# Optimization experiments

Measured on AMD Instinct MI355X. Metric: run time of the kernel, lower is better.

Reference implementation:

```python
import jax, jax.numpy as jnp
import numpy as np

N, E, D, ATT = 20000, 5000, 128, 32
NUM_LAYERS = 4
LN_EPS = 1e-5
DEG_EPS = 1e-12

def setup_inputs() -> dict:
    key = jax.random.key(0)
    k1, k2, k3, k4 = jax.random.split(key, 4)
    node_embeddings = jax.random.normal(k1, (N, D), dtype=jnp.float32)
    hypergraph_matrix = (jax.random.uniform(k2, (N, E)) < 0.01).astype(jnp.float32)
    ln_gamma = jnp.ones((D,), jnp.float32)
    ln_beta = jnp.zeros((D,), jnp.float32)
    W_att = jax.random.normal(k3, (D, ATT), dtype=jnp.float32) * (1.0 / np.sqrt(D))
    b_att = jnp.zeros((ATT,), jnp.float32)
    q_att = jax.random.normal(k4, (ATT,), dtype=jnp.float32)
    return {"node_embeddings": node_embeddings, "hypergraph_matrix": hypergraph_matrix,
            "ln_gamma": ln_gamma, "ln_beta": ln_beta,
            "W_att": W_att, "b_att": b_att, "q_att": q_att}

def _layernorm(y, gamma, beta):
    mu = jnp.mean(y, axis=-1, keepdims=True)
    var = jnp.mean(jnp.square(y - mu), axis=-1, keepdims=True)
    return (y - mu) * jax.lax.rsqrt(var + LN_EPS) * gamma + beta

def reference(node_embeddings, hypergraph_matrix, ln_gamma, ln_beta, W_att, b_att, q_att):
    H = hypergraph_matrix                      # [N, E]
    dv_inv = 1.0 / jnp.maximum(jnp.sum(H, axis=1), DEG_EPS)   # [N]
    de_inv = 1.0 / jnp.maximum(jnp.sum(H, axis=0), DEG_EPS)   # [E]
    x = node_embeddings
    for _ in range(NUM_LAYERS):
        edge_mean = (H.T @ x) * de_inv[:, None]       # V->E mean, [E, D]
        node_msg = (H @ edge_mean) * dv_inv[:, None]  # E->V mean, [N, D]
        x = _layernorm(node_msg + node_embeddings, ln_gamma, ln_beta)
        # dropout(p=0.35) is identity in eval mode
    # per-edge masked mean over member nodes (vectorized segment-mean)
    M = (H > 0).astype(x.dtype)                        # [N, E]
    cnt = jnp.maximum(jnp.sum(M, axis=0), 1.0)         # [E]
    edge_out = (M.T @ x) / cnt[:, None]                # [E, D]
    # dot-product attention pooling over hyperedges
    scores = jax.nn.softmax(jnp.tanh(edge_out @ W_att + b_att) @ q_att)  # [E]
    return scores @ edge_out                           # [D]
```

## Files before the change

kernel.cpp:

```cpp
#include <hip/hip_runtime.h>
#include <hip/hip_fp16.h>
#include <math.h>

#define NN 20000
#define EE 5000
#define DD 128
#define ATT 32
#define NUM_LAYERS 4
#define LN_EPS 1e-5f
#define DEG_EPS 1e-12f

#define ECAP 320
#define NCAP 128
#define CSTRIDE 32

typedef float vfloat4 __attribute__((ext_vector_type(4)));

__device__ inline unsigned pack2h(float x, float y) {
    return __builtin_bit_cast(unsigned, __floats2half2_rn(x, y));
}
__device__ inline void acc8(float* a, uint4 u) {
    __half2 h;
    h = __builtin_bit_cast(__half2, u.x); a[0] += __low2float(h); a[1] += __high2float(h);
    h = __builtin_bit_cast(__half2, u.y); a[2] += __low2float(h); a[3] += __high2float(h);
    h = __builtin_bit_cast(__half2, u.z); a[4] += __low2float(h); a[5] += __high2float(h);
    h = __builtin_bit_cast(__half2, u.w); a[6] += __low2float(h); a[7] += __high2float(h);
}

__global__ __launch_bounds__(256) void build_adj(
    const float* __restrict__ H, int* __restrict__ cur, int* __restrict__ nc,
    int* __restrict__ el, int* __restrict__ nl,
    const float* __restrict__ x0, __half* __restrict__ xh0) {
    const int n = blockIdx.x;
    const int tid = threadIdx.x;
    __shared__ int lcnt;
    __shared__ int lbuf[NCAP];
    if (tid == 0) lcnt = 0;
    __syncthreads();
    const vfloat4* row = reinterpret_cast<const vfloat4*>(H + (size_t)n * EE);
    for (int i = tid; i < EE / 4; i += 256) {
        const vfloat4 h = __builtin_nontemporal_load(row + i);
        float v[4] = {h.x, h.y, h.z, h.w};
        const int ebase = i * 4;
#pragma unroll
        for (int k = 0; k < 4; k++) {
            if (v[k] != 0.0f) {
                int s = atomicAdd(&lcnt, 1);
                if (s < NCAP) lbuf[s] = ebase + k;
            }
        }
    }
    __syncthreads();
    const int c = min(lcnt, NCAP);
    for (int k = tid; k < c; k += 256) {
        const int e = lbuf[k];
        nl[(size_t)n * NCAP + k] = e;
        const int slot = atomicAdd(&cur[e << 5], 1);
        if (slot < ECAP) el[(size_t)e * ECAP + slot] = n;
    }
    if (tid < 64) {
        const float2 v = reinterpret_cast<const float2*>(x0 + (size_t)n * DD)[tid];
        reinterpret_cast<unsigned*>(xh0 + (size_t)n * DD)[tid] = pack2h(v.x, v.y);
    }
    if (tid == 0) nc[n] = lcnt;
}

template <bool FINAL>
__global__ __launch_bounds__(256) void edge_gather16(
    const __half* __restrict__ xh, const int* __restrict__ cur,
    const int* __restrict__ el, __half* __restrict__ outh,
    float* __restrict__ eout, const float* __restrict__ W,
    const float* __restrict__ bb, const float* __restrict__ qv,
    float* __restrict__ t) {
    __shared__ int ilst[ECAP];
    __shared__ float part[4][16][8];
    __shared__ float rowbuf[DD];
    const int e = blockIdx.x;
    const int tid = threadIdx.x;
    const int cnt = cur[e << 5];
    const int c = min(cnt, ECAP);
    const int* lst = el + (size_t)e * ECAP;
    for (int k = tid; k < c; k += 256) ilst[k] = lst[k];
    __syncthreads();
    const int lane16 = tid & 15;
    const int s = tid >> 4;
    const int wave = tid >> 6;
    float a[8] = {0, 0, 0, 0, 0, 0, 0, 0};
    float b[8] = {0, 0, 0, 0, 0, 0, 0, 0};
    int i = s;
    for (; i + 48 < c; i += 64) {
        const int n0 = ilst[i];
        const int n1 = ilst[i + 16];
        const int n2 = ilst[i + 32];
        const int n3 = ilst[i + 48];
        const uint4 u0 = *reinterpret_cast<const uint4*>(xh + n0 * DD + lane16 * 8);
        const uint4 u1 = *reinterpret_cast<const uint4*>(xh + n1 * DD + lane16 * 8);
        const uint4 u2 = *reinterpret_cast<const uint4*>(xh + n2 * DD + lane16 * 8);
        const uint4 u3 = *reinterpret_cast<const uint4*>(xh + n3 * DD + lane16 * 8);
        acc8(a, u0); acc8(b, u1); acc8(a, u2); acc8(b, u3);
    }
    for (; i + 16 < c; i += 32) {
        const int n0 = ilst[i];
        const int n1 = ilst[i + 16];
        const uint4 u0 = *reinterpret_cast<const uint4*>(xh + n0 * DD + lane16 * 8);
        const uint4 u1 = *reinterpret_cast<const uint4*>(xh + n1 * DD + lane16 * 8);
        acc8(a, u0); acc8(b, u1);
    }
    if (i < c) {
        acc8(a, *reinterpret_cast<const uint4*>(xh + ilst[i] * DD + lane16 * 8));
    }
#pragma unroll
    for (int k = 0; k < 8; k++) {
        float v = a[k] + b[k];
        v += __shfl_down(v, 16);
        v += __shfl_down(v, 32);
        a[k] = v;
    }
    if ((tid & 63) < 16) {
#pragma unroll
        for (int k = 0; k < 8; k++) part[wave][lane16][k] = a[k];
    }
    __syncthreads();
    if (tid < 16) {
        const float inv = 1.0f / fmaxf((float)cnt, DEG_EPS);
        float o[8];
#pragma unroll
        for (int k = 0; k < 8; k++)
            o[k] = (part[0][tid][k] + part[1][tid][k] + part[2][tid][k] + part[3][tid][k]) * inv;
        if (!FINAL) {
            uint4 u;
            u.x = pack2h(o[0], o[1]); u.y = pack2h(o[2], o[3]);
            u.z = pack2h(o[4], o[5]); u.w = pack2h(o[6], o[7]);
            *reinterpret_cast<uint4*>(outh + e * DD + tid * 8) = u;
        } else {
#pragma unroll
            for (int k = 0; k < 8; k++) rowbuf[tid * 8 + k] = o[k];
            *reinterpret_cast<float4*>(eout + e * DD + tid * 8) =
                make_float4(o[0], o[1], o[2], o[3]);
            *reinterpret_cast<float4*>(eout + e * DD + tid * 8 + 4) =
                make_float4(o[4], o[5], o[6], o[7]);
        }
    }
    if (FINAL) {
        __syncthreads();
        float r = 0.0f;
        if (tid < ATT) {
            float acc = 0.0f;
#pragma unroll 4
            for (int d = 0; d < DD; d++) acc += rowbuf[d] * W[d * ATT + tid];
            r = tanhf(acc + bb[tid]) * qv[tid];
        }
        for (int off = 16; off > 0; off >>= 1) r += __shfl_down(r, off);
        if (tid == 0) t[e] = r;
    }
}

__global__ __launch_bounds__(128) void node_gather_ln16(
    const __half* __restrict__ emean, const int* __restrict__ nc,
    const int* __restrict__ nl, const float* __restrict__ x0,
    const float* __restrict__ gamma, const float* __restrict__ beta,
    __half* __restrict__ xout) {
    __shared__ int ilst[NCAP];
    __shared__ float part[2][16][8];
    const int n = blockIdx.x;
    const int tid = threadIdx.x;
    const int cnt = nc[n];
    const int c = min(cnt, NCAP);
    const int* lst = nl + (size_t)n * NCAP;
    if (tid < c) ilst[tid] = lst[tid];
    __syncthreads();
    const int lane16 = tid & 15;
    const int s = tid >> 4;
    const int wave = tid >> 6;
    float a[8] = {0, 0, 0, 0, 0, 0, 0, 0};
    float b[8] = {0, 0, 0, 0, 0, 0, 0, 0};
    int i = s;
    for (; i + 24 < c; i += 32) {
        const int e0 = ilst[i];
        const int e1 = ilst[i + 8];
        const int e2 = ilst[i + 16];
        const int e3 = ilst[i + 24];
        const uint4 u0 = *reinterpret_cast<const uint4*>(emean + e0 * DD + lane16 * 8);
        const uint4 u1 = *reinterpret_cast<const uint4*>(emean + e1 * DD + lane16 * 8);
        const uint4 u2 = *reinterpret_cast<const uint4*>(emean + e2 * DD + lane16 * 8);
        const uint4 u3 = *reinterpret_cast<const uint4*>(emean + e3 * DD + lane16 * 8);
        acc8(a, u0); acc8(b, u1); acc8(a, u2); acc8(b, u3);
    }
    for (; i + 8 < c; i += 16) {
        const int e0 = ilst[i];
        const int e1 = ilst[i + 8];
        const uint4 u0 = *reinterpret_cast<const uint4*>(emean + e0 * DD + lane16 * 8);
        const uint4 u1 = *reinterpret_cast<const uint4*>(emean + e1 * DD + lane16 * 8);
        acc8(a, u0); acc8(b, u1);
    }
    if (i < c) {
        acc8(a, *reinterpret_cast<const uint4*>(emean + ilst[i] * DD + lane16 * 8));
    }
#pragma unroll
    for (int k = 0; k < 8; k++) {
        float v = a[k] + b[k];
        v += __shfl_down(v, 16);
        v += __shfl_down(v, 32);
        a[k] = v;
    }
    if ((tid & 63) < 16) {
#pragma unroll
        for (int k = 0; k < 8; k++) part[wave][lane16][k] = a[k];
    }
    __syncthreads();
    if (tid < 16) {
        const float inv = 1.0f / fmaxf((float)cnt, DEG_EPS);
        const float4 x0a = *reinterpret_cast<const float4*>(x0 + n * DD + tid * 8);
        const float4 x0b = *reinterpret_cast<const float4*>(x0 + n * DD + tid * 8 + 4);
        float y[8];
        y[0] = (part[0][tid][0] + part[1][tid][0]) * inv + x0a.x;
        y[1] = (part[0][tid][1] + part[1][tid][1]) * inv + x0a.y;
        y[2] = (part[0][tid][2] + part[1][tid][2]) * inv + x0a.z;
        y[3] = (part[0][tid][3] + part[1][tid][3]) * inv + x0a.w;
        y[4] = (part[0][tid][4] + part[1][tid][4]) * inv + x0b.x;
        y[5] = (part[0][tid][5] + part[1][tid][5]) * inv + x0b.y;
        y[6] = (part[0][tid][6] + part[1][tid][6]) * inv + x0b.z;
        y[7] = (part[0][tid][7] + part[1][tid][7]) * inv + x0b.w;
        float sm = 0.0f, ss = 0.0f;
#pragma unroll
        for (int k = 0; k < 8; k++) { sm += y[k]; ss += y[k] * y[k]; }
        for (int off = 8; off > 0; off >>= 1) {
            sm += __shfl_down(sm, off);
            ss += __shfl_down(ss, off);
        }
        sm = __shfl(sm, 0);
        ss = __shfl(ss, 0);
        const float mu = sm * (1.0f / 128.0f);
        float var = ss * (1.0f / 128.0f) - mu * mu;
        var = fmaxf(var, 0.0f);
        const float rstd = 1.0f / sqrtf(var + LN_EPS);
        const float4 g0 = *reinterpret_cast<const float4*>(gamma + tid * 8);
        const float4 g1 = *reinterpret_cast<const float4*>(gamma + tid * 8 + 4);
        const float4 b0 = *reinterpret_cast<const float4*>(beta + tid * 8);
        const float4 b1 = *reinterpret_cast<const float4*>(beta + tid * 8 + 4);
        float gg[8] = {g0.x, g0.y, g0.z, g0.w, g1.x, g1.y, g1.z, g1.w};
        float bb[8] = {b0.x, b0.y, b0.z, b0.w, b1.x, b1.y, b1.z, b1.w};
        float o[8];
#pragma unroll
        for (int k = 0; k < 8; k++) o[k] = (y[k] - mu) * rstd * gg[k] + bb[k];
        uint4 u;
        u.x = pack2h(o[0], o[1]); u.y = pack2h(o[2], o[3]);
        u.z = pack2h(o[4], o[5]); u.w = pack2h(o[6], o[7]);
        *reinterpret_cast<uint4*>(xout + n * DD + tid * 8) = u;
    }
}

__global__ __launch_bounds__(1024) void softmax_stats(
    const float* __restrict__ t, float* __restrict__ MS) {
    __shared__ float red[16];
    __shared__ float smax;
    const int tid = threadIdx.x;
    const int wid = tid >> 6;
    float m = -1e30f;
    for (int i = tid; i < EE; i += 1024) m = fmaxf(m, t[i]);
    for (int off = 32; off > 0; off >>= 1) m = fmaxf(m, __shfl_down(m, off));
    if ((tid & 63) == 0) red[wid] = m;
    __syncthreads();
    if (tid < 64) {
        float v = (tid < 16) ? red[tid] : -1e30f;
        for (int off = 8; off > 0; off >>= 1) v = fmaxf(v, __shfl_down(v, off));
        if (tid == 0) smax = v;
    }
    __syncthreads();
    const float M = smax;
    float sum = 0.0f;
    for (int i = tid; i < EE; i += 1024) sum += expf(t[i] - M);
    for (int off = 32; off > 0; off >>= 1) sum += __shfl_down(sum, off);
    if ((tid & 63) == 0) red[wid] = sum;
    __syncthreads();
    if (tid < 64) {
        float v = (tid < 16) ? red[tid] : 0.0f;
        for (int off = 8; off > 0; off >>= 1) v += __shfl_down(v, off);
        if (tid == 0) { MS[0] = M; MS[1] = v; }
    }
}

__global__ __launch_bounds__(128) void weighted_sum(
    const float* __restrict__ eout, const float* __restrict__ t,
    const float* __restrict__ MS, float* __restrict__ out) {
    const int d = threadIdx.x;
    const float M = MS[0];
    const float invS = 1.0f / MS[1];
    float acc = 0.0f;
    for (int e = blockIdx.x; e < EE; e += gridDim.x) {
        const float w = expf(t[e] - M);
        acc += w * eout[e * DD + d];
    }
    atomicAdd(&out[d], acc * invS);
}

extern "C" void kernel_launch(void* const* d_in, const int* in_sizes, int n_in,
                              void* d_out, int out_size, void* d_ws, size_t ws_size,
                              hipStream_t stream) {
    const float* x0 = (const float*)d_in[0];
    const float* H = (const float*)d_in[1];
    const float* gamma = (const float*)d_in[2];
    const float* beta = (const float*)d_in[3];
    const float* W = (const float*)d_in[4];
    const float* b = (const float*)d_in[5];
    const float* qv = (const float*)d_in[6];
    float* out = (float*)d_out;

    char* w = (char*)d_ws;
    int* cur = (int*)w;       w += (size_t)EE * CSTRIDE * 4;
    int* nc = (int*)w;        w += (size_t)NN * 4;
    int* el = (int*)w;        w += (size_t)EE * ECAP * 4;
    int* nl = (int*)w;        w += (size_t)NN * NCAP * 4;
    __half* xh0 = (__half*)w; w += (size_t)NN * DD * 2;
    __half* xA = (__half*)w;  w += (size_t)NN * DD * 2;
    __half* xB = (__half*)w;  w += (size_t)NN * DD * 2;
    __half* emean = (__half*)w; w += (size_t)EE * DD * 2;
    float* eout = (float*)w;  w += (size_t)EE * DD * 4;
    float* t = (float*)w;     w += (size_t)EE * 4;
    float* MS = (float*)w;    w += 16;

    hipMemsetAsync(cur, 0, (size_t)EE * CSTRIDE * 4, stream);
    hipMemsetAsync(d_out, 0, (size_t)DD * sizeof(float), stream);

    build_adj<<<NN, 256, 0, stream>>>(H, cur, nc, el, nl, x0, xh0);

    const __half* xin = xh0;
    __half* bufs[2] = {xA, xB};
    for (int l = 0; l < NUM_LAYERS; l++) {
        edge_gather16<false><<<EE, 256, 0, stream>>>(
            xin, cur, el, emean, nullptr, nullptr, nullptr, nullptr, nullptr);
        node_gather_ln16<<<NN, 128, 0, stream>>>(
            emean, nc, nl, x0, gamma, beta, bufs[l & 1]);
        xin = bufs[l & 1];
    }

    edge_gather16<true><<<EE, 256, 0, stream>>>(
        xin, cur, el, nullptr, eout, W, b, qv, t);
    softmax_stats<<<1, 1024, 0, stream>>>(t, MS);
    weighted_sum<<<256, 128, 0, stream>>>(eout, t, MS, out);
}
```

Baseline: 730.6 us.

## Fuse all stages into one persistent cooperative kernel with grid syncs

Replaces the chain of roughly 12 kernel launches (adjacency build, four edge/node gather layers, final edge pass, softmax stats, weighted sum) with a single persistent cooperative kernel. The stages are separated by grid.sync and each block walks its work with a grid-stride loop. The intent is to remove per-launch overhead and the gaps between kernels. The trade-offs are grid-wide barrier cost, a grid capped at 1024 blocks with fewer waves in flight, and a serial softmax step on block 0. The old multi-kernel path is kept as a fallback if the cooperative launch fails.

```diff
diff --git a/kernel.cpp b/kernel.cpp
--- a/kernel.cpp
+++ b/kernel.cpp
@@ -1,6 +1,9 @@
 #include <hip/hip_runtime.h>
 #include <hip/hip_fp16.h>
+#include <hip/hip_cooperative_groups.h>
 #include <math.h>
+
+namespace cg = cooperative_groups;
 
 #define NN 20000
 #define EE 5000
@@ -25,6 +28,296 @@
     h = __builtin_bit_cast(__half2, u.y); a[2] += __low2float(h); a[3] += __high2float(h);
     h = __builtin_bit_cast(__half2, u.z); a[4] += __low2float(h); a[5] += __high2float(h);
     h = __builtin_bit_cast(__half2, u.w); a[6] += __low2float(h); a[7] += __high2float(h);
+}
+
+
+template <bool FINAL>
+__device__ __forceinline__ void edge_phase(
+    const __half* __restrict__ xh, const int* __restrict__ cur,
+    const int* __restrict__ el, __half* __restrict__ outh,
+    float* __restrict__ eout, const float* __restrict__ W,
+    const float* __restrict__ bb, const float* __restrict__ qv,
+    float* __restrict__ t, int* ilst, float (*part)[16][8], float* rowbuf) {
+    const int tid = threadIdx.x;
+    const int lane16 = tid & 15;
+    const int s = tid >> 4;
+    const int wave = tid >> 6;
+    for (int e = blockIdx.x; e < EE; e += gridDim.x) {
+        __syncthreads();
+        const int cnt = cur[e << 5];
+        const int c = min(cnt, ECAP);
+        const int* lst = el + (size_t)e * ECAP;
+        for (int k = tid; k < c; k += 256) ilst[k] = lst[k];
+        __syncthreads();
+        float a[8] = {0, 0, 0, 0, 0, 0, 0, 0};
+        float b[8] = {0, 0, 0, 0, 0, 0, 0, 0};
+        int i = s;
+        for (; i + 48 < c; i += 64) {
+            const int n0 = ilst[i];
+            const int n1 = ilst[i + 16];
+            const int n2 = ilst[i + 32];
+            const int n3 = ilst[i + 48];
+            const uint4 u0 = *reinterpret_cast<const uint4*>(xh + n0 * DD + lane16 * 8);
+            const uint4 u1 = *reinterpret_cast<const uint4*>(xh + n1 * DD + lane16 * 8);
+            const uint4 u2 = *reinterpret_cast<const uint4*>(xh + n2 * DD + lane16 * 8);
+            const uint4 u3 = *reinterpret_cast<const uint4*>(xh + n3 * DD + lane16 * 8);
+            acc8(a, u0); acc8(b, u1); acc8(a, u2); acc8(b, u3);
+        }
+        for (; i + 16 < c; i += 32) {
+            const int n0 = ilst[i];
+            const int n1 = ilst[i + 16];
+            const uint4 u0 = *reinterpret_cast<const uint4*>(xh + n0 * DD + lane16 * 8);
+            const uint4 u1 = *reinterpret_cast<const uint4*>(xh + n1 * DD + lane16 * 8);
+            acc8(a, u0); acc8(b, u1);
+        }
+        if (i < c) {
+            acc8(a, *reinterpret_cast<const uint4*>(xh + ilst[i] * DD + lane16 * 8));
+        }
+#pragma unroll
+        for (int k = 0; k < 8; k++) {
+            float v = a[k] + b[k];
+            v += __shfl_down(v, 16);
+            v += __shfl_down(v, 32);
+            a[k] = v;
+        }
+        if ((tid & 63) < 16) {
+#pragma unroll
+            for (int k = 0; k < 8; k++) part[wave][lane16][k] = a[k];
+        }
+        __syncthreads();
+        if (tid < 16) {
+            const float inv = 1.0f / fmaxf((float)cnt, DEG_EPS);
+            float o[8];
+#pragma unroll
+            for (int k = 0; k < 8; k++)
+                o[k] = (part[0][tid][k] + part[1][tid][k] + part[2][tid][k] + part[3][tid][k]) * inv;
+            if (!FINAL) {
+                uint4 u;
+                u.x = pack2h(o[0], o[1]); u.y = pack2h(o[2], o[3]);
+                u.z = pack2h(o[4], o[5]); u.w = pack2h(o[6], o[7]);
+                *reinterpret_cast<uint4*>(outh + e * DD + tid * 8) = u;
+            } else {
+#pragma unroll
+                for (int k = 0; k < 8; k++) rowbuf[tid * 8 + k] = o[k];
+                *reinterpret_cast<float4*>(eout + e * DD + tid * 8) =
+                    make_float4(o[0], o[1], o[2], o[3]);
+                *reinterpret_cast<float4*>(eout + e * DD + tid * 8 + 4) =
+                    make_float4(o[4], o[5], o[6], o[7]);
+            }
+        }
+        if (FINAL) {
+            __syncthreads();
+            float r = 0.0f;
+            if (tid < ATT) {
+                float acc = 0.0f;
+#pragma unroll 4
+                for (int d = 0; d < DD; d++) acc += rowbuf[d] * W[d * ATT + tid];
+                r = tanhf(acc + bb[tid]) * qv[tid];
+            }
+            for (int off = 16; off > 0; off >>= 1) r += __shfl_down(r, off);
+            if (tid == 0) t[e] = r;
+        }
+    }
+}
+
+__global__ __launch_bounds__(256, 4) void mega(
+    const float* __restrict__ x0, const float* __restrict__ H,
+    const float* __restrict__ gamma, const float* __restrict__ beta,
+    const float* __restrict__ W, const float* __restrict__ bb,
+    const float* __restrict__ qv,
+    int* __restrict__ cur, int* __restrict__ nc,
+    int* __restrict__ el, int* __restrict__ nl,
+    __half* __restrict__ xh0, __half* __restrict__ xA, __half* __restrict__ xB,
+    __half* __restrict__ emean, float* __restrict__ eout,
+    float* __restrict__ t, float* __restrict__ MS, float* __restrict__ out) {
+    cg::grid_group grid = cg::this_grid();
+    const int tid = threadIdx.x;
+
+    __shared__ int s_ilst[ECAP];
+    __shared__ float s_part[4][16][8];
+    __shared__ float s_rowbuf[DD];
+    __shared__ int s_lcnt;
+
+    for (int n = blockIdx.x; n < NN; n += gridDim.x) {
+        __syncthreads();
+        if (tid == 0) s_lcnt = 0;
+        __syncthreads();
+        const vfloat4* row = reinterpret_cast<const vfloat4*>(H + (size_t)n * EE);
+        for (int i = tid; i < EE / 4; i += 256) {
+            const vfloat4 h = __builtin_nontemporal_load(row + i);
+            float v[4] = {h.x, h.y, h.z, h.w};
+            const int ebase = i * 4;
+#pragma unroll
+            for (int k = 0; k < 4; k++) {
+                if (v[k] != 0.0f) {
+                    int sl = atomicAdd(&s_lcnt, 1);
+                    if (sl < NCAP) s_ilst[sl] = ebase + k;
+                }
+            }
+        }
+        __syncthreads();
+        const int cnt = s_lcnt;
+        const int c = min(cnt, NCAP);
+        for (int k = tid; k < c; k += 256) {
+            const int e = s_ilst[k];
+            nl[(size_t)n * NCAP + k] = e;
+            const int slot = atomicAdd(&cur[e << 5], 1);
+            if (slot < ECAP) el[(size_t)e * ECAP + slot] = n;
+        }
+        if (tid < 64) {
+            const float2 v = reinterpret_cast<const float2*>(x0 + (size_t)n * DD)[tid];
+            reinterpret_cast<unsigned*>(xh0 + (size_t)n * DD)[tid] = pack2h(v.x, v.y);
+        }
+        if (tid == 0) nc[n] = cnt;
+    }
+    grid.sync();
+
+    const __half* xin = xh0;
+    for (int l = 0; l < NUM_LAYERS; l++) {
+        edge_phase<false>(xin, cur, el, emean, nullptr, nullptr, nullptr, nullptr,
+                          nullptr, s_ilst, s_part, s_rowbuf);
+        grid.sync();
+
+        {
+            int (*nilst)[NCAP] = reinterpret_cast<int (*)[NCAP]>(s_ilst);
+            float (*npart)[2][16][8] = reinterpret_cast<float (*)[2][16][8]>(s_part);
+            __half* xout = (l & 1) ? xB : xA;
+            const int half = tid >> 7;
+            const int ltid = tid & 127;
+            const int lane16 = ltid & 15;
+            const int s = ltid >> 4;
+            const int wv = ltid >> 6;
+            for (int nb = blockIdx.x * 2; nb < NN; nb += gridDim.x * 2) {
+                const int n = nb + half;
+                __syncthreads();
+                const int cnt = nc[n];
+                const int c = min(cnt, NCAP);
+                const int* lst = nl + (size_t)n * NCAP;
+                if (ltid < c) nilst[half][ltid] = lst[ltid];
+                __syncthreads();
+                float a[8] = {0, 0, 0, 0, 0, 0, 0, 0};
+                float b[8] = {0, 0, 0, 0, 0, 0, 0, 0};
+                int i = s;
+                for (; i + 24 < c; i += 32) {
+                    const int e0 = nilst[half][i];
+                    const int e1 = nilst[half][i + 8];
+                    const int e2 = nilst[half][i + 16];
+                    const int e3 = nilst[half][i + 24];
+                    const uint4 u0 = *reinterpret_cast<const uint4*>(emean + e0 * DD + lane16 * 8);
+                    const uint4 u1 = *reinterpret_cast<const uint4*>(emean + e1 * DD + lane16 * 8);
+                    const uint4 u2 = *reinterpret_cast<const uint4*>(emean + e2 * DD + lane16 * 8);
+                    const uint4 u3 = *reinterpret_cast<const uint4*>(emean + e3 * DD + lane16 * 8);
+                    acc8(a, u0); acc8(b, u1); acc8(a, u2); acc8(b, u3);
+                }
+                for (; i + 8 < c; i += 16) {
+                    const int e0 = nilst[half][i];
+                    const int e1 = nilst[half][i + 8];
+                    const uint4 u0 = *reinterpret_cast<const uint4*>(emean + e0 * DD + lane16 * 8);
+                    const uint4 u1 = *reinterpret_cast<const uint4*>(emean + e1 * DD + lane16 * 8);
+                    acc8(a, u0); acc8(b, u1);
+                }
+                if (i < c) {
+                    acc8(a, *reinterpret_cast<const uint4*>(emean + nilst[half][i] * DD + lane16 * 8));
+                }
+#pragma unroll
+                for (int k = 0; k < 8; k++) {
+                    float v = a[k] + b[k];
+                    v += __shfl_down(v, 16);
+                    v += __shfl_down(v, 32);
+                    a[k] = v;
+                }
+                if ((ltid & 63) < 16) {
+#pragma unroll
+                    for (int k = 0; k < 8; k++) npart[half][wv][lane16][k] = a[k];
+                }
+                __syncthreads();
+                if (ltid < 16) {
+                    const float inv = 1.0f / fmaxf((float)cnt, DEG_EPS);
+                    const float4 x0a = *reinterpret_cast<const float4*>(x0 + n * DD + ltid * 8);
+                    const float4 x0b = *reinterpret_cast<const float4*>(x0 + n * DD + ltid * 8 + 4);
+                    float y[8];
+                    y[0] = (npart[half][0][ltid][0] + npart[half][1][ltid][0]) * inv + x0a.x;
+                    y[1] = (npart[half][0][ltid][1] + npart[half][1][ltid][1]) * inv + x0a.y;
+                    y[2] = (npart[half][0][ltid][2] + npart[half][1][ltid][2]) * inv + x0a.z;
+                    y[3] = (npart[half][0][ltid][3] + npart[half][1][ltid][3]) * inv + x0a.w;
+                    y[4] = (npart[half][0][ltid][4] + npart[half][1][ltid][4]) * inv + x0b.x;
+                    y[5] = (npart[half][0][ltid][5] + npart[half][1][ltid][5]) * inv + x0b.y;
+                    y[6] = (npart[half][0][ltid][6] + npart[half][1][ltid][6]) * inv + x0b.z;
+                    y[7] = (npart[half][0][ltid][7] + npart[half][1][ltid][7]) * inv + x0b.w;
+                    float sm = 0.0f, ss = 0.0f;
+#pragma unroll
+                    for (int k = 0; k < 8; k++) { sm += y[k]; ss += y[k] * y[k]; }
+                    for (int off = 8; off > 0; off >>= 1) {
+                        sm += __shfl_down(sm, off);
+                        ss += __shfl_down(ss, off);
+                    }
+                    sm = __shfl(sm, 0);
+                    ss = __shfl(ss, 0);
+                    const float mu = sm * (1.0f / 128.0f);
+                    float var = ss * (1.0f / 128.0f) - mu * mu;
+                    var = fmaxf(var, 0.0f);
+                    const float rstd = 1.0f / sqrtf(var + LN_EPS);
+                    const float4 g0 = *reinterpret_cast<const float4*>(gamma + ltid * 8);
+                    const float4 g1 = *reinterpret_cast<const float4*>(gamma + ltid * 8 + 4);
+                    const float4 b0 = *reinterpret_cast<const float4*>(beta + ltid * 8);
+                    const float4 b1 = *reinterpret_cast<const float4*>(beta + ltid * 8 + 4);
+                    float gg[8] = {g0.x, g0.y, g0.z, g0.w, g1.x, g1.y, g1.z, g1.w};
+                    float bv[8] = {b0.x, b0.y, b0.z, b0.w, b1.x, b1.y, b1.z, b1.w};
+                    float o[8];
+#pragma unroll
+                    for (int k = 0; k < 8; k++) o[k] = (y[k] - mu) * rstd * gg[k] + bv[k];
+                    uint4 u;
+                    u.x = pack2h(o[0], o[1]); u.y = pack2h(o[2], o[3]);
+                    u.z = pack2h(o[4], o[5]); u.w = pack2h(o[6], o[7]);
+                    *reinterpret_cast<uint4*>(xout + n * DD + ltid * 8) = u;
+                }
+            }
+        }
+        grid.sync();
+        xin = (l & 1) ? xB : xA;
+    }
+
+    edge_phase<true>(xin, cur, el, nullptr, eout, W, bb, qv, t,
+                     s_ilst, s_part, s_rowbuf);
+    grid.sync();
+
+    if (blockIdx.x == 0) {
+        __syncthreads();
+        float m = -1e30f;
+        for (int i = tid; i < EE; i += 256) m = fmaxf(m, t[i]);
+        for (int off = 32; off > 0; off >>= 1) m = fmaxf(m, __shfl_down(m, off));
+        if ((tid & 63) == 0) s_rowbuf[tid >> 6] = m;
+        __syncthreads();
+        if (tid == 0) {
+            s_rowbuf[8] = fmaxf(fmaxf(s_rowbuf[0], s_rowbuf[1]),
+                                fmaxf(s_rowbuf[2], s_rowbuf[3]));
+        }
+        __syncthreads();
+        const float M = s_rowbuf[8];
+        float sum = 0.0f;
+        for (int i = tid; i < EE; i += 256) sum += expf(t[i] - M);
+        for (int off = 32; off > 0; off >>= 1) sum += __shfl_down(sum, off);
+        if ((tid & 63) == 0) s_rowbuf[16 + (tid >> 6)] = sum;
+        __syncthreads();
+        if (tid == 0) {
+            MS[0] = M;
+            MS[1] = s_rowbuf[16] + s_rowbuf[17] + s_rowbuf[18] + s_rowbuf[19];
+        }
+    }
+    grid.sync();
+
+    {
+        const int WS = min((int)gridDim.x, 256);
+        if (blockIdx.x < WS && tid < 128) {
+            const float M = MS[0];
+            const float invS = 1.0f / MS[1];
+            float acc = 0.0f;
+            for (int e = blockIdx.x; e < EE; e += WS) {
+                acc += expf(t[e] - M) * eout[e * DD + tid];
+            }
+            atomicAdd(&out[tid], acc * invS);
+        }
+    }
 }
 
 __global__ __launch_bounds__(256) void build_adj(
@@ -75,8 +368,8 @@
     __shared__ int ilst[ECAP];
     __shared__ float part[4][16][8];
     __shared__ float rowbuf[DD];
+    const int tid = threadIdx.x;
     const int e = blockIdx.x;
-    const int tid = threadIdx.x;
     const int cnt = cur[e << 5];
     const int c = min(cnt, ECAP);
     const int* lst = el + (size_t)e * ECAP;
@@ -322,20 +615,41 @@
     hipMemsetAsync(cur, 0, (size_t)EE * CSTRIDE * 4, stream);
     hipMemsetAsync(d_out, 0, (size_t)DD * sizeof(float), stream);
 
-    build_adj<<<NN, 256, 0, stream>>>(H, cur, nc, el, nl, x0, xh0);
-
-    const __half* xin = xh0;
-    __half* bufs[2] = {xA, xB};
-    for (int l = 0; l < NUM_LAYERS; l++) {
-        edge_gather16<false><<<EE, 256, 0, stream>>>(
-            xin, cur, el, emean, nullptr, nullptr, nullptr, nullptr, nullptr);
-        node_gather_ln16<<<NN, 128, 0, stream>>>(
-            emean, nc, nl, x0, gamma, beta, bufs[l & 1]);
-        xin = bufs[l & 1];
-    }
-
-    edge_gather16<true><<<EE, 256, 0, stream>>>(
-        xin, cur, el, nullptr, eout, W, b, qv, t);
-    softmax_stats<<<1, 1024, 0, stream>>>(t, MS);
-    weighted_sum<<<256, 128, 0, stream>>>(eout, t, MS, out);
-}
+    static int grid = 0;
+    if (grid == 0) {
+        int mb = 0;
+        if (hipOccupancyMaxActiveBlocksPerMultiprocessor(&mb, mega, 256, 0)
+                != hipSuccess || mb <= 0)
+            mb = 4;
+        grid = mb * 256;
+        if (grid > 1024) grid = 1024;
+        if (grid < 256) grid = 256;
+    }
+
+    void* args[] = {(void*)&x0, (void*)&H, (void*)&gamma, (void*)&beta,
+                    (void*)&W, (void*)&b, (void*)&qv,
+                    (void*)&cur, (void*)&nc, (void*)&el, (void*)&nl,
+                    (void*)&xh0, (void*)&xA, (void*)&xB,
+                    (void*)&emean, (void*)&eout, (void*)&t, (void*)&MS,
+                    (void*)&out};
+    hipError_t err = hipLaunchCooperativeKernel(
+        mega, dim3(grid), dim3(256), args, 0, stream);
+
+    if (err != hipSuccess) {
+        (void)hipGetLastError();
+        build_adj<<<NN, 256, 0, stream>>>(H, cur, nc, el, nl, x0, xh0);
+        const __half* xin = xh0;
+        __half* bufs[2] = {xA, xB};
+        for (int l = 0; l < NUM_LAYERS; l++) {
+            edge_gather16<false><<<EE, 256, 0, stream>>>(
+                xin, cur, el, emean, nullptr, nullptr, nullptr, nullptr, nullptr);
+            node_gather_ln16<<<NN, 128, 0, stream>>>(
+                emean, nc, nl, x0, gamma, beta, bufs[l & 1]);
+            xin = bufs[l & 1];
+        }
+        edge_gather16<true><<<EE, 256, 0, stream>>>(
+            xin, cur, el, nullptr, eout, W, b, qv, t);
+        softmax_stats<<<1, 1024, 0, stream>>>(t, MS);
+        weighted_sum<<<256, 128, 0, stream>>>(eout, t, MS, out);
+    }
+}
```

Result: slower. 1.730 ms (+136.8%).

## Split node features into lo/hi half planes and split edge gather per half

Applied to the files above, without the earlier changes.

Stores the fp16 node feature matrix as two separate planes of 64 columns each, written by build_adj and node_gather_ln16. The per-layer edge gather now launches twice as many blocks, each summing only one half of the feature columns over a smaller 1.6 MB plane, with blocks ordered so the two halves of neighbouring edges are interleaved. The aim is better L2 locality on the random gathers and more parallelism. In exchange, each block reloads the edge's member list, and every gathered row read is only 128 bytes.

```diff
diff --git a/kernel.cpp b/kernel.cpp
--- a/kernel.cpp
+++ b/kernel.cpp
@@ -27,10 +27,12 @@
     h = __builtin_bit_cast(__half2, u.w); a[6] += __low2float(h); a[7] += __high2float(h);
 }
 
+
 __global__ __launch_bounds__(256) void build_adj(
     const float* __restrict__ H, int* __restrict__ cur, int* __restrict__ nc,
     int* __restrict__ el, int* __restrict__ nl,
-    const float* __restrict__ x0, __half* __restrict__ xh0) {
+    const float* __restrict__ x0, __half* __restrict__ xlo0,
+    __half* __restrict__ xhi0) {
     const int n = blockIdx.x;
     const int tid = threadIdx.x;
     __shared__ int lcnt;
@@ -60,15 +62,88 @@
     }
     if (tid < 64) {
         const float2 v = reinterpret_cast<const float2*>(x0 + (size_t)n * DD)[tid];
-        reinterpret_cast<unsigned*>(xh0 + (size_t)n * DD)[tid] = pack2h(v.x, v.y);
+        const unsigned u = pack2h(v.x, v.y);
+        if (tid < 32)
+            reinterpret_cast<unsigned*>(xlo0 + (size_t)n * 64)[tid] = u;
+        else
+            reinterpret_cast<unsigned*>(xhi0 + (size_t)n * 64)[tid - 32] = u;
     }
     if (tid == 0) nc[n] = lcnt;
 }
 
-template <bool FINAL>
-__global__ __launch_bounds__(256) void edge_gather16(
-    const __half* __restrict__ xh, const int* __restrict__ cur,
-    const int* __restrict__ el, __half* __restrict__ outh,
+__global__ __launch_bounds__(256) void edge_gather_half(
+    const __half* __restrict__ xlo, const __half* __restrict__ xhi,
+    const int* __restrict__ cur, const int* __restrict__ el,
+    __half* __restrict__ emean) {
+    __shared__ int ilst[ECAP];
+    __shared__ float part[4][8][8];
+    const int b = blockIdx.x;
+    const int g = b & 7;
+    const int half = g >> 2;
+    const int e = (b >> 3) * 4 + (g & 3);
+    const int tid = threadIdx.x;
+    const int cnt = cur[e << 5];
+    const int c = min(cnt, ECAP);
+    const int* lst = el + (size_t)e * ECAP;
+    for (int k = tid; k < c; k += 256) ilst[k] = lst[k];
+    __syncthreads();
+    const __half* xt = half ? xhi : xlo;
+    const int lane8 = tid & 7;
+    const int s = tid >> 3;
+    const int wave = tid >> 6;
+    float a[8] = {0, 0, 0, 0, 0, 0, 0, 0};
+    float bacc[8] = {0, 0, 0, 0, 0, 0, 0, 0};
+    int i = s;
+    for (; i + 96 < c; i += 128) {
+        const int n0 = ilst[i];
+        const int n1 = ilst[i + 32];
+        const int n2 = ilst[i + 64];
+        const int n3 = ilst[i + 96];
+        const uint4 u0 = *reinterpret_cast<const uint4*>(xt + n0 * 64 + lane8 * 8);
+        const uint4 u1 = *reinterpret_cast<const uint4*>(xt + n1 * 64 + lane8 * 8);
+        const uint4 u2 = *reinterpret_cast<const uint4*>(xt + n2 * 64 + lane8 * 8);
+        const uint4 u3 = *reinterpret_cast<const uint4*>(xt + n3 * 64 + lane8 * 8);
+        acc8(a, u0); acc8(bacc, u1); acc8(a, u2); acc8(bacc, u3);
+    }
+    for (; i + 32 < c; i += 64) {
+        const int n0 = ilst[i];
+        const int n1 = ilst[i + 32];
+        const uint4 u0 = *reinterpret_cast<const uint4*>(xt + n0 * 64 + lane8 * 8);
+        const uint4 u1 = *reinterpret_cast<const uint4*>(xt + n1 * 64 + lane8 * 8);
+        acc8(a, u0); acc8(bacc, u1);
+    }
+    if (i < c) {
+        acc8(a, *reinterpret_cast<const uint4*>(xt + ilst[i] * 64 + lane8 * 8));
+    }
+#pragma unroll
+    for (int k = 0; k < 8; k++) {
+        float v = a[k] + bacc[k];
+        v += __shfl_down(v, 8);
+        v += __shfl_down(v, 16);
+        v += __shfl_down(v, 32);
+        a[k] = v;
+    }
+    if ((tid & 63) < 8) {
+#pragma unroll
+        for (int k = 0; k < 8; k++) part[wave][lane8][k] = a[k];
+    }
+    __syncthreads();
+    if (tid < 8) {
+        const float inv = 1.0f / fmaxf((float)cnt, DEG_EPS);
+        float o[8];
+#pragma unroll
+        for (int k = 0; k < 8; k++)
+            o[k] = (part[0][tid][k] + part[1][tid][k] + part[2][tid][k] + part[3][tid][k]) * inv;
+        uint4 u;
+        u.x = pack2h(o[0], o[1]); u.y = pack2h(o[2], o[3]);
+        u.z = pack2h(o[4], o[5]); u.w = pack2h(o[6], o[7]);
+        *reinterpret_cast<uint4*>(emean + (size_t)e * DD + half * 64 + tid * 8) = u;
+    }
+}
+
+__global__ __launch_bounds__(256) void edge_final(
+    const __half* __restrict__ xlo, const __half* __restrict__ xhi,
+    const int* __restrict__ cur, const int* __restrict__ el,
     float* __restrict__ eout, const float* __restrict__ W,
     const float* __restrict__ bb, const float* __restrict__ qv,
     float* __restrict__ t) {
@@ -85,6 +160,7 @@
     const int lane16 = tid & 15;
     const int s = tid >> 4;
     const int wave = tid >> 6;
+    const __half* base = ((lane16 < 8) ? xlo : xhi) + (lane16 & 7) * 8;
     float a[8] = {0, 0, 0, 0, 0, 0, 0, 0};
     float b[8] = {0, 0, 0, 0, 0, 0, 0, 0};
     int i = s;
@@ -93,21 +169,21 @@
         const int n1 = ilst[i + 16];
         const int n2 = ilst[i + 32];
         const int n3 = ilst[i + 48];
-        const uint4 u0 = *reinterpret_cast<const uint4*>(xh + n0 * DD + lane16 * 8);
-        const uint4 u1 = *reinterpret_cast<const uint4*>(xh + n1 * DD + lane16 * 8);
-        const uint4 u2 = *reinterpret_cast<const uint4*>(xh + n2 * DD + lane16 * 8);
-        const uint4 u3 = *reinterpret_cast<const uint4*>(xh + n3 * DD + lane16 * 8);
+        const uint4 u0 = *reinterpret_cast<const uint4*>(base + n0 * 64);
+        const uint4 u1 = *reinterpret_cast<const uint4*>(base + n1 * 64);
+        const uint4 u2 = *reinterpret_cast<const uint4*>(base + n2 * 64);
+        const uint4 u3 = *reinterpret_cast<const uint4*>(base + n3 * 64);
         acc8(a, u0); acc8(b, u1); acc8(a, u2); acc8(b, u3);
     }
     for (; i + 16 < c; i += 32) {
         const int n0 = ilst[i];
         const int n1 = ilst[i + 16];
-        const uint4 u0 = *reinterpret_cast<const uint4*>(xh + n0 * DD + lane16 * 8);
-        const uint4 u1 = *reinterpret_cast<const uint4*>(xh + n1 * DD + lane16 * 8);
+        const uint4 u0 = *reinterpret_cast<const uint4*>(base + n0 * 64);
+        const uint4 u1 = *reinterpret_cast<const uint4*>(base + n1 * 64);
         acc8(a, u0); acc8(b, u1);
     }
     if (i < c) {
-        acc8(a, *reinterpret_cast<const uint4*>(xh + ilst[i] * DD + lane16 * 8));
+        acc8(a, *reinterpret_cast<const uint4*>(base + ilst[i] * 64));
     }
 #pragma unroll
     for (int k = 0; k < 8; k++) {
@@ -127,39 +203,30 @@
 #pragma unroll
         for (int k = 0; k < 8; k++)
             o[k] = (part[0][tid][k] + part[1][tid][k] + part[2][tid][k] + part[3][tid][k]) * inv;
-        if (!FINAL) {
-            uint4 u;
-            u.x = pack2h(o[0], o[1]); u.y = pack2h(o[2], o[3]);
-            u.z = pack2h(o[4], o[5]); u.w = pack2h(o[6], o[7]);
-            *reinterpret_cast<uint4*>(outh + e * DD + tid * 8) = u;
-        } else {
-#pragma unroll
-            for (int k = 0; k < 8; k++) rowbuf[tid * 8 + k] = o[k];
-            *reinterpret_cast<float4*>(eout + e * DD + tid * 8) =
-                make_float4(o[0], o[1], o[2], o[3]);
-            *reinterpret_cast<float4*>(eout + e * DD + tid * 8 + 4) =
-                make_float4(o[4], o[5], o[6], o[7]);
-        }
-    }
-    if (FINAL) {
-        __syncthreads();
-        float r = 0.0f;
-        if (tid < ATT) {
-            float acc = 0.0f;
+#pragma unroll
+        for (int k = 0; k < 8; k++) rowbuf[tid * 8 + k] = o[k];
+        *reinterpret_cast<float4*>(eout + e * DD + tid * 8) =
+            make_float4(o[0], o[1], o[2], o[3]);
+        *reinterpret_cast<float4*>(eout + e * DD + tid * 8 + 4) =
+            make_float4(o[4], o[5], o[6], o[7]);
+    }
+    __syncthreads();
+    float r = 0.0f;
+    if (tid < ATT) {
+        float acc = 0.0f;
 #pragma unroll 4
-            for (int d = 0; d < DD; d++) acc += rowbuf[d] * W[d * ATT + tid];
-            r = tanhf(acc + bb[tid]) * qv[tid];
-        }
-        for (int off = 16; off > 0; off >>= 1) r += __shfl_down(r, off);
-        if (tid == 0) t[e] = r;
-    }
+        for (int d = 0; d < DD; d++) acc += rowbuf[d] * W[d * ATT + tid];
+        r = tanhf(acc + bb[tid]) * qv[tid];
+    }
+    for (int off = 16; off > 0; off >>= 1) r += __shfl_down(r, off);
+    if (tid == 0) t[e] = r;
 }
 
 __global__ __launch_bounds__(128) void node_gather_ln16(
     const __half* __restrict__ emean, const int* __restrict__ nc,
     const int* __restrict__ nl, const float* __restrict__ x0,
     const float* __restrict__ gamma, const float* __restrict__ beta,
-    __half* __restrict__ xout) {
+    __half* __restrict__ xlo, __half* __restrict__ xhi) {
     __shared__ int ilst[NCAP];
     __shared__ float part[2][16][8];
     const int n = blockIdx.x;
@@ -246,7 +313,9 @@
         uint4 u;
         u.x = pack2h(o[0], o[1]); u.y = pack2h(o[2], o[3]);
         u.z = pack2h(o[4], o[5]); u.w = pack2h(o[6], o[7]);
-        *reinterpret_cast<uint4*>(xout + n * DD + tid * 8) = u;
+        __half* dst = (tid < 8) ? (xlo + (size_t)n * 64 + tid * 8)
+                                : (xhi + (size_t)n * 64 + (tid - 8) * 8);
+        *reinterpret_cast<uint4*>(dst) = u;
     }
 }
 
@@ -311,9 +380,12 @@
     int* nc = (int*)w;        w += (size_t)NN * 4;
     int* el = (int*)w;        w += (size_t)EE * ECAP * 4;
     int* nl = (int*)w;        w += (size_t)NN * NCAP * 4;
-    __half* xh0 = (__half*)w; w += (size_t)NN * DD * 2;
-    __half* xA = (__half*)w;  w += (size_t)NN * DD * 2;
-    __half* xB = (__half*)w;  w += (size_t)NN * DD * 2;
+    __half* xlo0 = (__half*)w; w += (size_t)NN * 64 * 2;
+    __half* xhi0 = (__half*)w; w += (size_t)NN * 64 * 2;
+    __half* xloA = (__half*)w; w += (size_t)NN * 64 * 2;
+    __half* xhiA = (__half*)w; w += (size_t)NN * 64 * 2;
+    __half* xloB = (__half*)w; w += (size_t)NN * 64 * 2;
+    __half* xhiB = (__half*)w; w += (size_t)NN * 64 * 2;
     __half* emean = (__half*)w; w += (size_t)EE * DD * 2;
     float* eout = (float*)w;  w += (size_t)EE * DD * 4;
     float* t = (float*)w;     w += (size_t)EE * 4;
@@ -322,20 +394,21 @@
     hipMemsetAsync(cur, 0, (size_t)EE * CSTRIDE * 4, stream);
     hipMemsetAsync(d_out, 0, (size_t)DD * sizeof(float), stream);
 
-    build_adj<<<NN, 256, 0, stream>>>(H, cur, nc, el, nl, x0, xh0);
-
-    const __half* xin = xh0;
-    __half* bufs[2] = {xA, xB};
+    build_adj<<<NN, 256, 0, stream>>>(H, cur, nc, el, nl, x0, xlo0, xhi0);
+
+    const __half* inlo = xlo0;
+    const __half* inhi = xhi0;
+    __half* lob[2] = {xloA, xloB};
+    __half* hib[2] = {xhiA, xhiB};
     for (int l = 0; l < NUM_LAYERS; l++) {
-        edge_gather16<false><<<EE, 256, 0, stream>>>(
-            xin, cur, el, emean, nullptr, nullptr, nullptr, nullptr, nullptr);
+        edge_gather_half<<<2 * EE, 256, 0, stream>>>(inlo, inhi, cur, el, emean);
         node_gather_ln16<<<NN, 128, 0, stream>>>(
-            emean, nc, nl, x0, gamma, beta, bufs[l & 1]);
-        xin = bufs[l & 1];
-    }
-
-    edge_gather16<true><<<EE, 256, 0, stream>>>(
-        xin, cur, el, nullptr, eout, W, b, qv, t);
+            emean, nc, nl, x0, gamma, beta, lob[l & 1], hib[l & 1]);
+        inlo = lob[l & 1];
+        inhi = hib[l & 1];
+    }
+
+    edge_final<<<EE, 256, 0, stream>>>(inlo, inhi, cur, el, eout, W, b, qv, t);
     softmax_stats<<<1, 1024, 0, stream>>>(t, MS);
     weighted_sum<<<256, 128, 0, stream>>>(eout, t, MS, out);
 }
```

After: 742.1 us. Within noise of the previous version (+1.6%).

## Split fp16 node features into two 64-wide halves for cache-resident edge gathers

Applied to the files above, without the earlier changes.

Node features are stored as two separate 64-column fp16 arrays, and each edge gather runs twice, once per half. Each pass then touches only half the feature bytes, which should let its random-access working set stay in L2. The attention logits move out of the final edge gather into their own small kernel. Edge and node index lists are now loaded into shared memory unconditionally with nontemporal loads, and the node kernel writes the split arrays in place instead of ping-ponging buffers. In exchange, each layer launches one more kernel and reads the edge index lists twice.

```diff
diff --git a/kernel.cpp b/kernel.cpp
--- a/kernel.cpp
+++ b/kernel.cpp
@@ -27,10 +27,12 @@
     h = __builtin_bit_cast(__half2, u.w); a[6] += __low2float(h); a[7] += __high2float(h);
 }
 
+
 __global__ __launch_bounds__(256) void build_adj(
     const float* __restrict__ H, int* __restrict__ cur, int* __restrict__ nc,
     int* __restrict__ el, int* __restrict__ nl,
-    const float* __restrict__ x0, __half* __restrict__ xh0) {
+    const float* __restrict__ x0, __half* __restrict__ xlo,
+    __half* __restrict__ xhi) {
     const int n = blockIdx.x;
     const int tid = threadIdx.x;
     __shared__ int lcnt;
@@ -60,68 +62,71 @@
     }
     if (tid < 64) {
         const float2 v = reinterpret_cast<const float2*>(x0 + (size_t)n * DD)[tid];
-        reinterpret_cast<unsigned*>(xh0 + (size_t)n * DD)[tid] = pack2h(v.x, v.y);
+        const unsigned u = pack2h(v.x, v.y);
+        if (tid < 32)
+            reinterpret_cast<unsigned*>(xlo + (size_t)n * 64)[tid] = u;
+        else
+            reinterpret_cast<unsigned*>(xhi + (size_t)n * 64)[tid - 32] = u;
     }
     if (tid == 0) nc[n] = lcnt;
 }
 
 template <bool FINAL>
-__global__ __launch_bounds__(256) void edge_gather16(
-    const __half* __restrict__ xh, const int* __restrict__ cur,
-    const int* __restrict__ el, __half* __restrict__ outh,
-    float* __restrict__ eout, const float* __restrict__ W,
-    const float* __restrict__ bb, const float* __restrict__ qv,
-    float* __restrict__ t) {
+__global__ __launch_bounds__(256) void edge_half(
+    const __half* __restrict__ xt, const int* __restrict__ cur,
+    const int* __restrict__ el, __half* __restrict__ emean,
+    float* __restrict__ eout, int hoff) {
     __shared__ int ilst[ECAP];
-    __shared__ float part[4][16][8];
-    __shared__ float rowbuf[DD];
+    __shared__ float part[4][8][8];
     const int e = blockIdx.x;
     const int tid = threadIdx.x;
+    const int* lst = el + (size_t)e * ECAP;
+    ilst[tid] = __builtin_nontemporal_load(lst + tid);
+    if (tid < ECAP - 256) ilst[256 + tid] = __builtin_nontemporal_load(lst + 256 + tid);
     const int cnt = cur[e << 5];
     const int c = min(cnt, ECAP);
-    const int* lst = el + (size_t)e * ECAP;
-    for (int k = tid; k < c; k += 256) ilst[k] = lst[k];
-    __syncthreads();
-    const int lane16 = tid & 15;
-    const int s = tid >> 4;
+    __syncthreads();
+    const int lane8 = tid & 7;
+    const int s = tid >> 3;
     const int wave = tid >> 6;
     float a[8] = {0, 0, 0, 0, 0, 0, 0, 0};
-    float b[8] = {0, 0, 0, 0, 0, 0, 0, 0};
+    float bacc[8] = {0, 0, 0, 0, 0, 0, 0, 0};
     int i = s;
-    for (; i + 48 < c; i += 64) {
+    for (; i + 96 < c; i += 128) {
         const int n0 = ilst[i];
-        const int n1 = ilst[i + 16];
-        const int n2 = ilst[i + 32];
-        const int n3 = ilst[i + 48];
-        const uint4 u0 = *reinterpret_cast<const uint4*>(xh + n0 * DD + lane16 * 8);
-        const uint4 u1 = *reinterpret_cast<const uint4*>(xh + n1 * DD + lane16 * 8);
-        const uint4 u2 = *reinterpret_cast<const uint4*>(xh + n2 * DD + lane16 * 8);
-        const uint4 u3 = *reinterpret_cast<const uint4*>(xh + n3 * DD + lane16 * 8);
-        acc8(a, u0); acc8(b, u1); acc8(a, u2); acc8(b, u3);
-    }
-    for (; i + 16 < c; i += 32) {
+        const int n1 = ilst[i + 32];
+        const int n2 = ilst[i + 64];
+        const int n3 = ilst[i + 96];
+        const uint4 u0 = *reinterpret_cast<const uint4*>(xt + n0 * 64 + lane8 * 8);
+        const uint4 u1 = *reinterpret_cast<const uint4*>(xt + n1 * 64 + lane8 * 8);
+        const uint4 u2 = *reinterpret_cast<const uint4*>(xt + n2 * 64 + lane8 * 8);
+        const uint4 u3 = *reinterpret_cast<const uint4*>(xt + n3 * 64 + lane8 * 8);
+        acc8(a, u0); acc8(bacc, u1); acc8(a, u2); acc8(bacc, u3);
+    }
+    for (; i + 32 < c; i += 64) {
         const int n0 = ilst[i];
-        const int n1 = ilst[i + 16];
-        const uint4 u0 = *reinterpret_cast<const uint4*>(xh + n0 * DD + lane16 * 8);
-        const uint4 u1 = *reinterpret_cast<const uint4*>(xh + n1 * DD + lane16 * 8);
-        acc8(a, u0); acc8(b, u1);
+        const int n1 = ilst[i + 32];
+        const uint4 u0 = *reinterpret_cast<const uint4*>(xt + n0 * 64 + lane8 * 8);
+        const uint4 u1 = *reinterpret_cast<const uint4*>(xt + n1 * 64 + lane8 * 8);
+        acc8(a, u0); acc8(bacc, u1);
     }
     if (i < c) {
-        acc8(a, *reinterpret_cast<const uint4*>(xh + ilst[i] * DD + lane16 * 8));
+        acc8(a, *reinterpret_cast<const uint4*>(xt + ilst[i] * 64 + lane8 * 8));
     }
 #pragma unroll
     for (int k = 0; k < 8; k++) {
-        float v = a[k] + b[k];
+        float v = a[k] + bacc[k];
+        v += __shfl_down(v, 8);
         v += __shfl_down(v, 16);
         v += __shfl_down(v, 32);
         a[k] = v;
     }
-    if ((tid & 63) < 16) {
-#pragma unroll
-        for (int k = 0; k < 8; k++) part[wave][lane16][k] = a[k];
-    }
-    __syncthreads();
-    if (tid < 16) {
+    if ((tid & 63) < 8) {
+#pragma unroll
+        for (int k = 0; k < 8; k++) part[wave][lane8][k] = a[k];
+    }
+    __syncthreads();
+    if (tid < 8) {
         const float inv = 1.0f / fmaxf((float)cnt, DEG_EPS);
         float o[8];
 #pragma unroll
@@ -131,43 +136,51 @@
             uint4 u;
             u.x = pack2h(o[0], o[1]); u.y = pack2h(o[2], o[3]);
             u.z = pack2h(o[4], o[5]); u.w = pack2h(o[6], o[7]);
-            *reinterpret_cast<uint4*>(outh + e * DD + tid * 8) = u;
+            *reinterpret_cast<uint4*>(emean + (size_t)e * DD + hoff + tid * 8) = u;
         } else {
-#pragma unroll
-            for (int k = 0; k < 8; k++) rowbuf[tid * 8 + k] = o[k];
-            *reinterpret_cast<float4*>(eout + e * DD + tid * 8) =
+            *reinterpret_cast<float4*>(eout + (size_t)e * DD + hoff + tid * 8) =
                 make_float4(o[0], o[1], o[2], o[3]);
-            *reinterpret_cast<float4*>(eout + e * DD + tid * 8 + 4) =
+            *reinterpret_cast<float4*>(eout + (size_t)e * DD + hoff + tid * 8 + 4) =
                 make_float4(o[4], o[5], o[6], o[7]);
         }
     }
-    if (FINAL) {
-        __syncthreads();
-        float r = 0.0f;
-        if (tid < ATT) {
-            float acc = 0.0f;
+}
+
+__global__ __launch_bounds__(64) void logits(
+    const float* __restrict__ eout, const float* __restrict__ W,
+    const float* __restrict__ bb, const float* __restrict__ qv,
+    float* __restrict__ t) {
+    __shared__ float rowbuf[DD];
+    const int e = blockIdx.x;
+    const int tid = threadIdx.x;
+    const float2 v = reinterpret_cast<const float2*>(eout + (size_t)e * DD)[tid];
+    rowbuf[tid * 2] = v.x;
+    rowbuf[tid * 2 + 1] = v.y;
+    __syncthreads();
+    float r = 0.0f;
+    if (tid < ATT) {
+        float acc = 0.0f;
 #pragma unroll 4
-            for (int d = 0; d < DD; d++) acc += rowbuf[d] * W[d * ATT + tid];
-            r = tanhf(acc + bb[tid]) * qv[tid];
-        }
-        for (int off = 16; off > 0; off >>= 1) r += __shfl_down(r, off);
-        if (tid == 0) t[e] = r;
-    }
+        for (int d = 0; d < DD; d++) acc += rowbuf[d] * W[d * ATT + tid];
+        r = tanhf(acc + bb[tid]) * qv[tid];
+    }
+    for (int off = 16; off > 0; off >>= 1) r += __shfl_down(r, off);
+    if (tid == 0) t[e] = r;
 }
 
 __global__ __launch_bounds__(128) void node_gather_ln16(
     const __half* __restrict__ emean, const int* __restrict__ nc,
     const int* __restrict__ nl, const float* __restrict__ x0,
     const float* __restrict__ gamma, const float* __restrict__ beta,
-    __half* __restrict__ xout) {
+    __half* __restrict__ xlo, __half* __restrict__ xhi) {
     __shared__ int ilst[NCAP];
     __shared__ float part[2][16][8];
     const int n = blockIdx.x;
     const int tid = threadIdx.x;
+    const int* lst = nl + (size_t)n * NCAP;
+    ilst[tid] = __builtin_nontemporal_load(lst + tid);
     const int cnt = nc[n];
     const int c = min(cnt, NCAP);
-    const int* lst = nl + (size_t)n * NCAP;
-    if (tid < c) ilst[tid] = lst[tid];
     __syncthreads();
     const int lane16 = tid & 15;
     const int s = tid >> 4;
@@ -246,7 +259,9 @@
         uint4 u;
         u.x = pack2h(o[0], o[1]); u.y = pack2h(o[2], o[3]);
         u.z = pack2h(o[4], o[5]); u.w = pack2h(o[6], o[7]);
-        *reinterpret_cast<uint4*>(xout + n * DD + tid * 8) = u;
+        __half* dst = (tid < 8) ? (xlo + (size_t)n * 64 + tid * 8)
+                                : (xhi + (size_t)n * 64 + (tid - 8) * 8);
+        *reinterpret_cast<uint4*>(dst) = u;
     }
 }
 
@@ -311,9 +326,8 @@
     int* nc = (int*)w;        w += (size_t)NN * 4;
     int* el = (int*)w;        w += (size_t)EE * ECAP * 4;
     int* nl = (int*)w;        w += (size_t)NN * NCAP * 4;
-    __half* xh0 = (__half*)w; w += (size_t)NN * DD * 2;
-    __half* xA = (__half*)w;  w += (size_t)NN * DD * 2;
-    __half* xB = (__half*)w;  w += (size_t)NN * DD * 2;
+    __half* xlo = (__half*)w; w += (size_t)NN * 64 * 2;
+    __half* xhi = (__half*)w; w += (size_t)NN * 64 * 2;
     __half* emean = (__half*)w; w += (size_t)EE * DD * 2;
     float* eout = (float*)w;  w += (size_t)EE * DD * 4;
     float* t = (float*)w;     w += (size_t)EE * 4;
@@ -322,20 +336,18 @@
     hipMemsetAsync(cur, 0, (size_t)EE * CSTRIDE * 4, stream);
     hipMemsetAsync(d_out, 0, (size_t)DD * sizeof(float), stream);
 
-    build_adj<<<NN, 256, 0, stream>>>(H, cur, nc, el, nl, x0, xh0);
-
-    const __half* xin = xh0;
-    __half* bufs[2] = {xA, xB};
+    build_adj<<<NN, 256, 0, stream>>>(H, cur, nc, el, nl, x0, xlo, xhi);
+
     for (int l = 0; l < NUM_LAYERS; l++) {
-        edge_gather16<false><<<EE, 256, 0, stream>>>(
-            xin, cur, el, emean, nullptr, nullptr, nullptr, nullptr, nullptr);
+        edge_half<false><<<EE, 256, 0, stream>>>(xlo, cur, el, emean, nullptr, 0);
+        edge_half<false><<<EE, 256, 0, stream>>>(xhi, cur, el, emean, nullptr, 64);
         node_gather_ln16<<<NN, 128, 0, stream>>>(
-            emean, nc, nl, x0, gamma, beta, bufs[l & 1]);
-        xin = bufs[l & 1];
-    }
-
-    edge_gather16<true><<<EE, 256, 0, stream>>>(
-        xin, cur, el, nullptr, eout, W, b, qv, t);
+            emean, nc, nl, x0, gamma, beta, xlo, xhi);
+    }
+
+    edge_half<true><<<EE, 256, 0, stream>>>(xlo, cur, el, nullptr, eout, 0);
+    edge_half<true><<<EE, 256, 0, stream>>>(xhi, cur, el, nullptr, eout, 64);
+    logits<<<EE, 64, 0, stream>>>(eout, W, b, qv, t);
     softmax_stats<<<1, 1024, 0, stream>>>(t, MS);
     weighted_sum<<<256, 128, 0, stream>>>(eout, t, MS, out);
 }
```

After: 790.0 us. 8.1% more time.
